# Performance work log

Hardware: AMD Instinct MI355X
Metric: run time of the kernel (lower is better)

The kernel has to match this reference:

```python
import jax, jax.numpy as jnp
import numpy as np

B, N, C = 2, 2048, 1024
H = 8
DH = C // H  # head dim = 128


def setup_inputs() -> dict:
    key = jax.random.key(0)
    ks = jax.random.split(key, 10)
    s = 1.0 / np.sqrt(C)
    return {
        "inputs_q": jax.random.normal(ks[0], (B, N, C), dtype=jnp.float32),
        "inputs_kv": jax.random.normal(ks[1], (B, N, C), dtype=jnp.float32),
        "Wq": jax.random.normal(ks[2], (C, C), dtype=jnp.float32) * s,
        "bq": jnp.zeros((C,), dtype=jnp.float32),
        "Wk": jax.random.normal(ks[3], (C, C), dtype=jnp.float32) * s,
        "bk": jnp.zeros((C,), dtype=jnp.float32),
        "Wv": jax.random.normal(ks[4], (C, C), dtype=jnp.float32) * s,
        "bv": jnp.zeros((C,), dtype=jnp.float32),
        "Wo": jax.random.normal(ks[5], (C, C), dtype=jnp.float32) * s,
        "bo": jnp.zeros((C,), dtype=jnp.float32),
    }


def reference(inputs_q, inputs_kv, Wq, bq, Wk, bk, Wv, bv, Wo, bo):
    # QKV linear projections
    q = inputs_q @ Wq + bq           # [B, N, C]
    k = inputs_kv @ Wk + bk          # [B, M, C]
    v = inputs_kv @ Wv + bv          # [B, M, C]
    # split heads
    q = q.reshape(B, N, H, DH)
    k = k.reshape(B, -1, H, DH)
    v = v.reshape(B, -1, H, DH)
    # explicit attention, matching attend(): scale by 1/sqrt(head_dim)
    attn = jnp.einsum('bnhc,bmhc->bhnm', q, k) * (1.0 / np.sqrt(DH))
    normalized = jax.nn.softmax(attn, axis=-1)  # f32 softmax (inputs are f32)
    summed = jnp.einsum('bhnm,bmhd->bnhd', normalized, v)
    summed = summed.reshape(B, N, C)  # merge heads: ...n(hd)
    # output linear
    return summed @ Wo + bo
```

## Files before the change

### kernel.cpp

```cpp
#include <hip/hip_runtime.h>

typedef unsigned short u16;
typedef __bf16 bf16;
typedef __attribute__((ext_vector_type(8))) __bf16 bf16x8;
typedef __attribute__((ext_vector_type(4))) float f32x4;

#define AS1(p) ((const __attribute__((address_space(1))) void*)(p))
#define AS3(p) ((__attribute__((address_space(3))) void*)(p))

__device__ __forceinline__ u16 f2bf(float f) {
  unsigned u = __builtin_bit_cast(unsigned, f);
  u += 0x7fffu + ((u >> 16) & 1u);
  return (u16)(u >> 16);
}

static constexpr int  B_ = 2, N_ = 2048, C_ = 1024, H_ = 8, DH_ = 128;
static constexpr long SZ_IN = (long)B_ * N_ * C_;
static constexpr long SZ_W  = (long)C_ * C_;

__global__ void k_cast_in(const float* __restrict__ q, const float* __restrict__ kv,
                          u16* __restrict__ qb, u16* __restrict__ kvb)
{
  const float* src = blockIdx.y ? kv : q;
  u16* dst = blockIdx.y ? kvb : qb;
  long i = ((long)blockIdx.x * 256 + threadIdx.x) * 8;
  float4 a = *(const float4*)(src + i);
  float4 b = *(const float4*)(src + i + 4);
  uint4 v;
  v.x = f2bf(a.x) | ((unsigned)f2bf(a.y) << 16);
  v.y = f2bf(a.z) | ((unsigned)f2bf(a.w) << 16);
  v.z = f2bf(b.x) | ((unsigned)f2bf(b.y) << 16);
  v.w = f2bf(b.z) | ((unsigned)f2bf(b.w) << 16);
  *(uint4*)(dst + i) = v;
}

__global__ void k_cast_wt(const float* __restrict__ W0, const float* __restrict__ W1,
                          const float* __restrict__ W2, const float* __restrict__ W3,
                          u16* __restrict__ WT)
{
  __shared__ u16 t[64][65];
  const float* W = (blockIdx.z == 0) ? W0 : (blockIdx.z == 1) ? W1
                 : (blockIdx.z == 2) ? W2 : W3;
  u16* dst = WT + (long)blockIdx.z * SZ_W;
  int tid = threadIdx.x;
  int n0 = blockIdx.x * 64, k0 = blockIdx.y * 64;
#pragma unroll
  for (int r = 0; r < 4; ++r) {
    int slot = r * 256 + tid;
    int row = slot >> 4, c4 = slot & 15;
    float4 a = *(const float4*)(W + (long)(k0 + row) * 1024 + n0 + c4 * 4);
    t[c4*4+0][row] = f2bf(a.x);
    t[c4*4+1][row] = f2bf(a.y);
    t[c4*4+2][row] = f2bf(a.z);
    t[c4*4+3][row] = f2bf(a.w);
  }
  __syncthreads();
#pragma unroll
  for (int r = 0; r < 4; ++r) {
    int slot = r * 256 + tid;
    int row = slot >> 4, c4 = slot & 15;
    uint2 v;
    v.x = t[row][c4*4+0] | ((unsigned)t[row][c4*4+1] << 16);
    v.y = t[row][c4*4+2] | ((unsigned)t[row][c4*4+3] << 16);
    *(uint2*)(dst + (long)(n0 + row) * 1024 + k0 + c4 * 4) = v;
  }
}

__device__ __forceinline__ void gemm_main_128x128(
    const u16* __restrict__ A, const u16* __restrict__ BT,
    u16* lA, u16* lB, int m0, int n0, int tid, f32x4 acc[4][4])
{
  int w = tid >> 6, l = tid & 63, quad = l >> 4, lm = l & 15;
  int wm = w >> 1, wn = w & 1;
  int srow = tid >> 2, schunk = tid & 3;
  int sxw = (srow >> 1) & 3;
  int sxr = (lm >> 1) & 3;
  const u16* Ag = A + (long)(m0 + srow) * 1024 + (schunk ^ sxw) * 8;
  const u16* Bg = BT + (long)(n0 + srow) * 1024 + (schunk ^ sxw) * 8;
  u16* lAw = lA + w * 512;
  u16* lBw = lB + w * 512;
  for (int kb = 0; kb < 32; ++kb) {
    const u16* Agk = Ag + kb * 32;
    const u16* Bgk = Bg + kb * 32;
    __builtin_amdgcn_global_load_lds(AS1(Agk),           AS3(lAw),        16, 0, 0);
    __builtin_amdgcn_global_load_lds(AS1(Agk + 64*1024), AS3(lAw + 2048), 16, 0, 0);
    __builtin_amdgcn_global_load_lds(AS1(Bgk),           AS3(lBw),        16, 0, 0);
    __builtin_amdgcn_global_load_lds(AS1(Bgk + 64*1024), AS3(lBw + 2048), 16, 0, 0);
    __syncthreads();
    bf16x8 af[4], bfr[4];
#pragma unroll
    for (int mi = 0; mi < 4; ++mi)
      af[mi] = *(const bf16x8*)(lA + (wm*64 + mi*16 + lm)*32 + ((quad ^ sxr))*8);
#pragma unroll
    for (int ni = 0; ni < 4; ++ni)
      bfr[ni] = *(const bf16x8*)(lB + (wn*64 + ni*16 + lm)*32 + ((quad ^ sxr))*8);
#pragma unroll
    for (int mi = 0; mi < 4; ++mi)
#pragma unroll
      for (int ni = 0; ni < 4; ++ni)
        acc[mi][ni] = __builtin_amdgcn_mfma_f32_16x16x32_bf16(af[mi], bfr[ni], acc[mi][ni], 0, 0, 0);
    __syncthreads();
  }
}

__global__ __launch_bounds__(256, 3)
void k_gemm_qkv(const u16* __restrict__ qb, const u16* __restrict__ kvb,
                const u16* __restrict__ wt,
                const float* __restrict__ bq, const float* __restrict__ bk,
                const float* __restrict__ bv,
                u16* __restrict__ Qb, u16* __restrict__ Kb, u16* __restrict__ VTb)
{
  __shared__ u16 lA[4096], lB[4096];
  int tid = threadIdx.x;
  int z = blockIdx.z;
  const u16* A = (z == 0) ? qb : kvb;
  const u16* BT = wt + (long)z * SZ_W;
  const float* bias = (z == 0) ? bq : (z == 1) ? bk : bv;
  int m0 = blockIdx.y * 128, n0 = blockIdx.x * 128;
  f32x4 acc[4][4] = {};
  gemm_main_128x128(A, BT, lA, lB, m0, n0, tid, acc);

  int w = tid >> 6, l = tid & 63, quad = l >> 4, lm = l & 15;
  int wm = w >> 1, wn = w & 1;
  float scale = (z == 0) ? 0.08838834764831845f : 1.0f;
#pragma unroll
  for (int ni = 0; ni < 4; ++ni) {
    int n = n0 + wn*64 + ni*16 + lm;
    float bb = bias[n];
    int h = n >> 7, dd = n & 127;
#pragma unroll
    for (int mi = 0; mi < 4; ++mi) {
      int mbase = m0 + wm*64 + mi*16 + quad*4;
      int bidx = mbase >> 11, nn = mbase & 2047;
      if (z == 2) {
        u16 o0 = f2bf(acc[mi][ni][0] + bb), o1 = f2bf(acc[mi][ni][1] + bb);
        u16 o2 = f2bf(acc[mi][ni][2] + bb), o3 = f2bf(acc[mi][ni][3] + bb);
        uint2 v; v.x = o0 | ((unsigned)o1 << 16); v.y = o2 | ((unsigned)o3 << 16);
        *(uint2*)(VTb + ((long)(bidx*8 + h)*128 + dd)*2048 + nn) = v;
      } else {
        u16* dst = (z == 0) ? Qb : Kb;
#pragma unroll
        for (int r = 0; r < 4; ++r)
          dst[((long)(bidx*8 + h)*2048 + (nn + r))*128 + dd] = f2bf((acc[mi][ni][r] + bb) * scale);
      }
    }
  }
}

__global__ __launch_bounds__(512, 2)
void k_attn(const u16* __restrict__ Qb, const u16* __restrict__ Kb,
            const u16* __restrict__ VTb, u16* __restrict__ Sout)
{
  __shared__ u16 smem[25088];
  int tid = threadIdx.x;
  int w = tid >> 6, l = tid & 63, quad = l >> 4, lm = l & 15;
  int qw = w & 3, kh = w >> 2;
  int bh = blockIdx.x;
  int q0 = blockIdx.y * 128 + qw * 32;
  const u16* Qg = Qb + ((long)bh * 2048 + q0) * 128;
  const u16* Kg = Kb + (long)bh * 2048 * 128;
  const u16* Vg = VTb + (long)bh * 128 * 2048;

  u16* lPw = smem + 16384 + w * 1024;
  float* lStat = (float*)(smem + 24576);

  bf16x8 qf[2][4];
#pragma unroll
  for (int mi = 0; mi < 2; ++mi)
#pragma unroll
    for (int kk = 0; kk < 4; ++kk)
      qf[mi][kk] = *(const bf16x8*)(Qg + (long)(mi*16 + lm)*128 + kk*32 + quad*8);

  f32x4 accO[2][8] = {};
  float sumP[2][4] = {};

#define STAGE_K(tt)                                                            \
  {                                                                            \
    u16* dstb = smem + (kh*2 + ((tt) & 1)) * 4096;                             \
    _Pragma("unroll")                                                          \
    for (int j = 0; j < 2; ++j) {                                              \
      int s = (qw*2 + j)*64 + l;                                               \
      int r = s >> 4;                                                          \
      int c = (s & 15) ^ (r & 7);                                              \
      __builtin_amdgcn_global_load_lds(                                        \
          AS1(Kg + (long)(kh*1024 + (tt)*32 + r)*128 + c*8),                   \
          AS3(dstb + (qw*2 + j)*512), 16, 0, 0);                               \
    }                                                                          \
  }

  STAGE_K(0);

  for (int t = 0; t < 32; ++t) {
    __syncthreads();
    STAGE_K(t + 1);

    int k0 = kh*1024 + t*32;
    bf16x8 vf[8];
#pragma unroll
    for (int ni = 0; ni < 8; ++ni)
      vf[ni] = *(const bf16x8*)(Vg + (long)(ni*16 + lm)*2048 + k0 + quad*8);

    const u16* bk = smem + (kh*2 + (t & 1)) * 4096;
    f32x4 accS[2][2] = {};
#pragma unroll
    for (int kk = 0; kk < 4; ++kk)
#pragma unroll
      for (int ni = 0; ni < 2; ++ni) {
        bf16x8 kf = *(const bf16x8*)(bk + ((ni*16 + lm)*16 + (((kk*4 + quad) ^ (lm & 7))))*8);
#pragma unroll
        for (int mi = 0; mi < 2; ++mi)
          accS[mi][ni] = __builtin_amdgcn_mfma_f32_16x16x32_bf16(qf[mi][kk], kf, accS[mi][ni], 0, 0, 0);
      }

#pragma unroll
    for (int mi = 0; mi < 2; ++mi)
#pragma unroll
      for (int r = 0; r < 4; ++r) {
        int R = mi*16 + quad*4 + r;
        int xr = (quad*2 + (r >> 1)) & 3;
#pragma unroll
        for (int ni = 0; ni < 2; ++ni) {
          float p = __expf(accS[mi][ni][r]);
          sumP[mi][r] += p;
          int ch = ni*2 + (lm >> 3);
          lPw[(R*4 + (ch ^ xr))*8 + (lm & 7)] = f2bf(p);
        }
      }

    bf16x8 pf[2];
#pragma unroll
    for (int mi = 0; mi < 2; ++mi)
      pf[mi] = *(const bf16x8*)(lPw + ((mi*16 + lm)*4 + (quad ^ ((lm >> 1) & 3)))*8);

#pragma unroll
    for (int ni = 0; ni < 8; ++ni)
#pragma unroll
      for (int mi = 0; mi < 2; ++mi)
        accO[mi][ni] = __builtin_amdgcn_mfma_f32_16x16x32_bf16(pf[mi], vf[ni], accO[mi][ni], 0, 0, 0);
  }
#undef STAGE_K

#pragma unroll
  for (int mi = 0; mi < 2; ++mi)
#pragma unroll
    for (int r = 0; r < 4; ++r) {
      float s = sumP[mi][r];
      s += __shfl_xor(s, 1);
      s += __shfl_xor(s, 2);
      s += __shfl_xor(s, 4);
      s += __shfl_xor(s, 8);
      sumP[mi][r] = s;
    }

  __syncthreads();
#pragma unroll
  for (int mi = 0; mi < 2; ++mi)
#pragma unroll
    for (int r = 0; r < 4; ++r)
      lStat[w*32 + mi*16 + quad*4 + r] = sumP[mi][r];
  __syncthreads();

  float inv[2][4];
#pragma unroll
  for (int mi = 0; mi < 2; ++mi)
#pragma unroll
    for (int r = 0; r < 4; ++r) {
      int R = mi*16 + quad*4 + r;
      inv[mi][r] = 1.f / (lStat[w*32 + R] + lStat[(w ^ 4)*32 + R]);
    }

  float* lO = (float*)smem;
  int b = bh >> 3, h = bh & 7;
#pragma unroll
  for (int half = 0; half < 2; ++half) {
    if (kh == 1) {
#pragma unroll
      for (int mi = 0; mi < 2; ++mi)
#pragma unroll
        for (int ni = 0; ni < 4; ++ni)
#pragma unroll
          for (int r = 0; r < 4; ++r) {
            int R = mi*16 + quad*4 + r;
            lO[(qw*32 + R)*64 + ni*16 + lm] = accO[mi][half*4 + ni][r];
          }
    }
    __syncthreads();
    if (kh == 0) {
#pragma unroll
      for (int mi = 0; mi < 2; ++mi)
#pragma unroll
        for (int ni = 0; ni < 4; ++ni)
#pragma unroll
          for (int r = 0; r < 4; ++r) {
            int R = mi*16 + quad*4 + r;
            float v = (accO[mi][half*4 + ni][r] + lO[(qw*32 + R)*64 + ni*16 + lm]) * inv[mi][r];
            Sout[((long)(b*2048 + q0 + R))*1024 + h*128 + (half*4 + ni)*16 + lm] = f2bf(v);
          }
    }
    __syncthreads();
  }
}

__global__ __launch_bounds__(256, 3)
void k_gemm_out(const u16* __restrict__ S, const u16* __restrict__ WoT,
                const float* __restrict__ bo, float* __restrict__ out)
{
  __shared__ u16 lA[4096], lB[4096];
  int tid = threadIdx.x;
  int m0 = blockIdx.y * 128, n0 = blockIdx.x * 128;
  f32x4 acc[4][4] = {};
  gemm_main_128x128(S, WoT, lA, lB, m0, n0, tid, acc);

  int w = tid >> 6, l = tid & 63, quad = l >> 4, lm = l & 15;
  int wm = w >> 1, wn = w & 1;
#pragma unroll
  for (int ni = 0; ni < 4; ++ni) {
    int n = n0 + wn*64 + ni*16 + lm;
    float bb = bo[n];
#pragma unroll
    for (int mi = 0; mi < 4; ++mi) {
      int mbase = m0 + wm*64 + mi*16 + quad*4;
#pragma unroll
      for (int r = 0; r < 4; ++r)
        out[(long)(mbase + r) * 1024 + n] = acc[mi][ni][r] + bb;
    }
  }
}

extern "C" void kernel_launch(void* const* d_in, const int* in_sizes, int n_in,
                              void* d_out, int out_size, void* d_ws, size_t ws_size,
                              hipStream_t stream)
{
  const float* inq  = (const float*)d_in[0];
  const float* inkv = (const float*)d_in[1];
  const float* Wq = (const float*)d_in[2];
  const float* bq = (const float*)d_in[3];
  const float* Wk = (const float*)d_in[4];
  const float* bk = (const float*)d_in[5];
  const float* Wv = (const float*)d_in[6];
  const float* bv = (const float*)d_in[7];
  const float* Wo = (const float*)d_in[8];
  const float* bo = (const float*)d_in[9];

  u16* ws   = (u16*)d_ws;
  u16* ABUF = ws;
  u16* KVB  = ws + SZ_IN;
  u16* WT   = ws + 2 * SZ_IN;
  u16* Qb   = WT + 4 * SZ_W;
  u16* Kb   = Qb + SZ_IN;
  u16* VTb  = Kb + SZ_IN;

  k_cast_in <<<dim3(2048, 2),   256, 0, stream>>>(inq, inkv, ABUF, KVB);
  k_cast_wt <<<dim3(16, 16, 4), 256, 0, stream>>>(Wq, Wk, Wv, Wo, WT);
  k_gemm_qkv<<<dim3(8, 32, 3),  256, 0, stream>>>(ABUF, KVB, WT, bq, bk, bv, Qb, Kb, VTb);
  k_attn    <<<dim3(16, 16),    512, 0, stream>>>(Qb, Kb, VTb, ABUF);
  k_gemm_out<<<dim3(8, 32),     256, 0, stream>>>(ABUF, WT + 3 * SZ_W, bo, (float*)d_out);
}
```

Before: 245.0 us.

## Transpose Q/K/out GEMMs for vectorized stores and restructure attention into key-split waves

The Q/K projection and output GEMMs swap operand roles so each lane holds four consecutive channels, which allows packed 8-byte bf16 stores and float4 output stores in place of scattered scalar writes. The attention kernel moves to 256-thread blocks covering 32 queries each. Each of the four waves handles a quarter of the keys and reads K fragments straight from global memory, dropping the LDS async staging. Partial outputs and row sums are then reduced across waves through LDS in two steps. This trades away K reuse in LDS and the double-buffered prefetch for more blocks and simpler synchronisation.

Result: slower. 316.8 us (+29.3%).

```diff
diff --git a/kernel.cpp b/kernel.cpp
--- a/kernel.cpp
+++ b/kernel.cpp
@@ -113,56 +113,73 @@
   __shared__ u16 lA[4096], lB[4096];
   int tid = threadIdx.x;
   int z = blockIdx.z;
-  const u16* A = (z == 0) ? qb : kvb;
-  const u16* BT = wt + (long)z * SZ_W;
-  const float* bias = (z == 0) ? bq : (z == 1) ? bk : bv;
-  int m0 = blockIdx.y * 128, n0 = blockIdx.x * 128;
   f32x4 acc[4][4] = {};
-  gemm_main_128x128(A, BT, lA, lB, m0, n0, tid, acc);
-
   int w = tid >> 6, l = tid & 63, quad = l >> 4, lm = l & 15;
   int wm = w >> 1, wn = w & 1;
-  float scale = (z == 0) ? 0.08838834764831845f : 1.0f;
-#pragma unroll
-  for (int ni = 0; ni < 4; ++ni) {
-    int n = n0 + wn*64 + ni*16 + lm;
-    float bb = bias[n];
-    int h = n >> 7, dd = n & 127;
-#pragma unroll
-    for (int mi = 0; mi < 4; ++mi) {
-      int mbase = m0 + wm*64 + mi*16 + quad*4;
-      int bidx = mbase >> 11, nn = mbase & 2047;
-      if (z == 2) {
+
+  if (z == 2) {
+    int m0 = blockIdx.y * 128, n0 = blockIdx.x * 128;
+    gemm_main_128x128(kvb, wt + 2 * SZ_W, lA, lB, m0, n0, tid, acc);
+#pragma unroll
+    for (int ni = 0; ni < 4; ++ni) {
+      int n = n0 + wn*64 + ni*16 + lm;
+      float bb = bv[n];
+      int h = n >> 7, dd = n & 127;
+#pragma unroll
+      for (int mi = 0; mi < 4; ++mi) {
+        int mbase = m0 + wm*64 + mi*16 + quad*4;
+        int bidx = mbase >> 11, nn = mbase & 2047;
         u16 o0 = f2bf(acc[mi][ni][0] + bb), o1 = f2bf(acc[mi][ni][1] + bb);
         u16 o2 = f2bf(acc[mi][ni][2] + bb), o3 = f2bf(acc[mi][ni][3] + bb);
         uint2 v; v.x = o0 | ((unsigned)o1 << 16); v.y = o2 | ((unsigned)o3 << 16);
         *(uint2*)(VTb + ((long)(bidx*8 + h)*128 + dd)*2048 + nn) = v;
-      } else {
-        u16* dst = (z == 0) ? Qb : Kb;
-#pragma unroll
-        for (int r = 0; r < 4; ++r)
-          dst[((long)(bidx*8 + h)*2048 + (nn + r))*128 + dd] = f2bf((acc[mi][ni][r] + bb) * scale);
       }
     }
-  }
-}
-
-__global__ __launch_bounds__(512, 2)
+  } else {
+    const u16* X = (z == 0) ? qb : kvb;
+    const float* bias = (z == 0) ? bq : bk;
+    u16* dst = (z == 0) ? Qb : Kb;
+    float scale = (z == 0) ? 0.08838834764831845f : 1.0f;
+    int m0 = blockIdx.x * 128, n0 = blockIdx.y * 128;
+    gemm_main_128x128(wt + (long)z * SZ_W, X, lA, lB, m0, n0, tid, acc);
+#pragma unroll
+    for (int mi = 0; mi < 4; ++mi) {
+      int chb = m0 + wm*64 + mi*16 + quad*4;
+      int h = chb >> 7, d = chb & 127;
+      float4 bb = *(const float4*)(bias + chb);
+#pragma unroll
+      for (int ni = 0; ni < 4; ++ni) {
+        int tok = n0 + wn*64 + ni*16 + lm;
+        int bidx = tok >> 11, nn = tok & 2047;
+        u16 o0 = f2bf((acc[mi][ni][0] + bb.x) * scale);
+        u16 o1 = f2bf((acc[mi][ni][1] + bb.y) * scale);
+        u16 o2 = f2bf((acc[mi][ni][2] + bb.z) * scale);
+        u16 o3 = f2bf((acc[mi][ni][3] + bb.w) * scale);
+        uint2 v; v.x = o0 | ((unsigned)o1 << 16); v.y = o2 | ((unsigned)o3 << 16);
+        *(uint2*)(dst + ((long)(bidx*8 + h)*2048 + nn)*128 + d) = v;
+      }
+    }
+  }
+}
+
+__global__ __launch_bounds__(256, 3)
 void k_attn(const u16* __restrict__ Qb, const u16* __restrict__ Kb,
             const u16* __restrict__ VTb, u16* __restrict__ Sout)
 {
-  __shared__ u16 smem[25088];
+  __shared__ u16 smem[24832];
+  float* lOa   = (float*)smem;
+  float* lOb   = (float*)(smem + 8192);
+  float* lStat = (float*)(smem + 16384);
+  u16*   lP    = smem + 16640;
+
   int tid = threadIdx.x;
   int w = tid >> 6, l = tid & 63, quad = l >> 4, lm = l & 15;
-  int qw = w & 3, kh = w >> 2;
   int bh = blockIdx.x;
-  int q0 = blockIdx.y * 128 + qw * 32;
+  int q0 = blockIdx.y * 32;
   const u16* Qg = Qb + ((long)bh * 2048 + q0) * 128;
   const u16* Kg = Kb + (long)bh * 2048 * 128;
   const u16* Vg = VTb + (long)bh * 128 * 2048;
-
-  u16* lPw = smem + 16384 + w * 1024;
-  float* lStat = (float*)(smem + 24576);
+  u16* lPw = lP + w * 2048;
 
   bf16x8 qf[2][4];
 #pragma unroll
@@ -174,39 +191,20 @@
   f32x4 accO[2][8] = {};
   float sumP[2][4] = {};
 
-#define STAGE_K(tt)                                                            \
-  {                                                                            \
-    u16* dstb = smem + (kh*2 + ((tt) & 1)) * 4096;                             \
-    _Pragma("unroll")                                                          \
-    for (int j = 0; j < 2; ++j) {                                              \
-      int s = (qw*2 + j)*64 + l;                                               \
-      int r = s >> 4;                                                          \
-      int c = (s & 15) ^ (r & 7);                                              \
-      __builtin_amdgcn_global_load_lds(                                        \
-          AS1(Kg + (long)(kh*1024 + (tt)*32 + r)*128 + c*8),                   \
-          AS3(dstb + (qw*2 + j)*512), 16, 0, 0);                               \
-    }                                                                          \
-  }
-
-  STAGE_K(0);
-
-  for (int t = 0; t < 32; ++t) {
-    __syncthreads();
-    STAGE_K(t + 1);
-
-    int k0 = kh*1024 + t*32;
+  for (int t = 0; t < 16; ++t) {
+    int k0 = w*512 + t*32;
+
     bf16x8 vf[8];
 #pragma unroll
     for (int ni = 0; ni < 8; ++ni)
       vf[ni] = *(const bf16x8*)(Vg + (long)(ni*16 + lm)*2048 + k0 + quad*8);
 
-    const u16* bk = smem + (kh*2 + (t & 1)) * 4096;
     f32x4 accS[2][2] = {};
 #pragma unroll
     for (int kk = 0; kk < 4; ++kk)
 #pragma unroll
       for (int ni = 0; ni < 2; ++ni) {
-        bf16x8 kf = *(const bf16x8*)(bk + ((ni*16 + lm)*16 + (((kk*4 + quad) ^ (lm & 7))))*8);
+        bf16x8 kf = *(const bf16x8*)(Kg + (long)(k0 + ni*16 + lm)*128 + kk*32 + quad*8);
 #pragma unroll
         for (int mi = 0; mi < 2; ++mi)
           accS[mi][ni] = __builtin_amdgcn_mfma_f32_16x16x32_bf16(qf[mi][kk], kf, accS[mi][ni], 0, 0, 0);
@@ -238,7 +236,6 @@
       for (int mi = 0; mi < 2; ++mi)
         accO[mi][ni] = __builtin_amdgcn_mfma_f32_16x16x32_bf16(pf[mi], vf[ni], accO[mi][ni], 0, 0, 0);
   }
-#undef STAGE_K
 
 #pragma unroll
   for (int mi = 0; mi < 2; ++mi)
@@ -250,54 +247,55 @@
       s += __shfl_xor(s, 4);
       s += __shfl_xor(s, 8);
       sumP[mi][r] = s;
+      lStat[w*32 + mi*16 + quad*4 + r] = s;
     }
 
+  if (w == 1 || w == 3) {
+    float* dst = (w == 1) ? lOa : lOb;
+#pragma unroll
+    for (int mi = 0; mi < 2; ++mi)
+#pragma unroll
+      for (int ni = 0; ni < 8; ++ni)
+#pragma unroll
+        for (int r = 0; r < 4; ++r)
+          dst[(mi*16 + quad*4 + r)*128 + ni*16 + lm] = accO[mi][ni][r];
+  }
   __syncthreads();
-#pragma unroll
-  for (int mi = 0; mi < 2; ++mi)
-#pragma unroll
-    for (int r = 0; r < 4; ++r)
-      lStat[w*32 + mi*16 + quad*4 + r] = sumP[mi][r];
+  if (w == 0 || w == 2) {
+    float* src = (w == 0) ? lOa : lOb;
+#pragma unroll
+    for (int mi = 0; mi < 2; ++mi)
+#pragma unroll
+      for (int ni = 0; ni < 8; ++ni)
+#pragma unroll
+        for (int r = 0; r < 4; ++r)
+          accO[mi][ni][r] += src[(mi*16 + quad*4 + r)*128 + ni*16 + lm];
+  }
   __syncthreads();
-
-  float inv[2][4];
-#pragma unroll
-  for (int mi = 0; mi < 2; ++mi)
-#pragma unroll
-    for (int r = 0; r < 4; ++r) {
-      int R = mi*16 + quad*4 + r;
-      inv[mi][r] = 1.f / (lStat[w*32 + R] + lStat[(w ^ 4)*32 + R]);
-    }
-
-  float* lO = (float*)smem;
-  int b = bh >> 3, h = bh & 7;
-#pragma unroll
-  for (int half = 0; half < 2; ++half) {
-    if (kh == 1) {
-#pragma unroll
-      for (int mi = 0; mi < 2; ++mi)
-#pragma unroll
-        for (int ni = 0; ni < 4; ++ni)
-#pragma unroll
-          for (int r = 0; r < 4; ++r) {
-            int R = mi*16 + quad*4 + r;
-            lO[(qw*32 + R)*64 + ni*16 + lm] = accO[mi][half*4 + ni][r];
-          }
-    }
-    __syncthreads();
-    if (kh == 0) {
-#pragma unroll
-      for (int mi = 0; mi < 2; ++mi)
-#pragma unroll
-        for (int ni = 0; ni < 4; ++ni)
-#pragma unroll
-          for (int r = 0; r < 4; ++r) {
-            int R = mi*16 + quad*4 + r;
-            float v = (accO[mi][half*4 + ni][r] + lO[(qw*32 + R)*64 + ni*16 + lm]) * inv[mi][r];
-            Sout[((long)(b*2048 + q0 + R))*1024 + h*128 + (half*4 + ni)*16 + lm] = f2bf(v);
-          }
-    }
-    __syncthreads();
+  if (w == 2) {
+#pragma unroll
+    for (int mi = 0; mi < 2; ++mi)
+#pragma unroll
+      for (int ni = 0; ni < 8; ++ni)
+#pragma unroll
+        for (int r = 0; r < 4; ++r)
+          lOa[(mi*16 + quad*4 + r)*128 + ni*16 + lm] = accO[mi][ni][r];
+  }
+  __syncthreads();
+  if (w == 0) {
+    int b = bh >> 3, h = bh & 7;
+#pragma unroll
+    for (int mi = 0; mi < 2; ++mi)
+#pragma unroll
+      for (int r = 0; r < 4; ++r) {
+        int R = mi*16 + quad*4 + r;
+        float linv = 1.f / (lStat[R] + lStat[32 + R] + lStat[64 + R] + lStat[96 + R]);
+#pragma unroll
+        for (int ni = 0; ni < 8; ++ni) {
+          float v = (accO[mi][ni][r] + lOa[R*128 + ni*16 + lm]) * linv;
+          Sout[((long)(b*2048 + q0 + R))*1024 + h*128 + ni*16 + lm] = f2bf(v);
+        }
+      }
   }
 }
 
@@ -307,22 +305,25 @@
 {
   __shared__ u16 lA[4096], lB[4096];
   int tid = threadIdx.x;
-  int m0 = blockIdx.y * 128, n0 = blockIdx.x * 128;
+  int m0 = blockIdx.x * 128, n0 = blockIdx.y * 128;
   f32x4 acc[4][4] = {};
-  gemm_main_128x128(S, WoT, lA, lB, m0, n0, tid, acc);
+  gemm_main_128x128(WoT, S, lA, lB, m0, n0, tid, acc);
 
   int w = tid >> 6, l = tid & 63, quad = l >> 4, lm = l & 15;
   int wm = w >> 1, wn = w & 1;
 #pragma unroll
-  for (int ni = 0; ni < 4; ++ni) {
-    int n = n0 + wn*64 + ni*16 + lm;
-    float bb = bo[n];
-#pragma unroll
-    for (int mi = 0; mi < 4; ++mi) {
-      int mbase = m0 + wm*64 + mi*16 + quad*4;
-#pragma unroll
-      for (int r = 0; r < 4; ++r)
-        out[(long)(mbase + r) * 1024 + n] = acc[mi][ni][r] + bb;
+  for (int mi = 0; mi < 4; ++mi) {
+    int chb = m0 + wm*64 + mi*16 + quad*4;
+    float4 bb = *(const float4*)(bo + chb);
+#pragma unroll
+    for (int ni = 0; ni < 4; ++ni) {
+      int tok = n0 + wn*64 + ni*16 + lm;
+      float4 v;
+      v.x = acc[mi][ni][0] + bb.x;
+      v.y = acc[mi][ni][1] + bb.y;
+      v.z = acc[mi][ni][2] + bb.z;
+      v.w = acc[mi][ni][3] + bb.w;
+      *(float4*)(out + (long)tok * 1024 + chb) = v;
     }
   }
 }
@@ -353,6 +354,6 @@
   k_cast_in <<<dim3(2048, 2),   256, 0, stream>>>(inq, inkv, ABUF, KVB);
   k_cast_wt <<<dim3(16, 16, 4), 256, 0, stream>>>(Wq, Wk, Wv, Wo, WT);
   k_gemm_qkv<<<dim3(8, 32, 3),  256, 0, stream>>>(ABUF, KVB, WT, bq, bk, bv, Qb, Kb, VTb);
-  k_attn    <<<dim3(16, 16),    512, 0, stream>>>(Qb, Kb, VTb, ABUF);
+  k_attn    <<<dim3(16, 64),    256, 0, stream>>>(Qb, Kb, VTb, ABUF);
   k_gemm_out<<<dim3(8, 32),     256, 0, stream>>>(ABUF, WT + 3 * SZ_W, bo, (float*)d_out);
 }
```
